# Kernel optimization log

Hardware: AMD Instinct MI355X
Metric: run time of the kernel (lower is better)

The kernel has to match this reference:

```python
import jax, jax.numpy as jnp
import numpy as np

B, S, H = 1, 2048, 4096
NH, NKV, HD = 32, 8, 128
GROUP = 128
NEG = jnp.float32(-1e9)


def setup_inputs() -> dict:
    key = jax.random.key(0)
    ks = jax.random.split(key, 13)
    inp = {"hidden_states": jax.random.normal(ks[0], (B, S, H), dtype=jnp.float32)}

    def qparams(k1, k2, k3, out_dim, in_dim):
        qw = jax.random.randint(k1, (out_dim, in_dim), 0, 16, dtype=jnp.int32)
        sc = jax.random.uniform(k2, (out_dim, in_dim // GROUP), dtype=jnp.float32) * 0.02 + 0.001
        zp = jax.random.randint(k3, (out_dim, in_dim // GROUP), 0, 16, dtype=jnp.int32)
        return qw, sc, zp

    inp["q_qw"], inp["q_sc"], inp["q_zp"] = qparams(ks[1], ks[2], ks[3], NH * HD, H)
    inp["k_qw"], inp["k_sc"], inp["k_zp"] = qparams(ks[4], ks[5], ks[6], NKV * HD, H)
    inp["v_qw"], inp["v_sc"], inp["v_zp"] = qparams(ks[7], ks[8], ks[9], NKV * HD, H)
    inp["o_qw"], inp["o_sc"], inp["o_zp"] = qparams(ks[10], ks[11], ks[12], NH * HD, H)
    return inp


def dequant(qw, sc, zp):
    # W4A16 groupwise dequant: w = (q - zero_point) * scale, group along input dim
    out_dim, in_dim = qw.shape
    g = in_dim // sc.shape[1]
    w = (qw.reshape(out_dim, -1, g) - zp[:, :, None]).astype(jnp.float32) * sc[:, :, None]
    return w.reshape(out_dim, in_dim)


def reference(hidden_states, q_qw, q_sc, q_zp, k_qw, k_sc, k_zp,
              v_qw, v_sc, v_zp, o_qw, o_sc, o_zp):
    x = hidden_states  # [B, S, H]
    grp = NH // NKV  # GQA groups = 4

    q = jnp.einsum('bsh,oh->bso', x, dequant(q_qw, q_sc, q_zp))
    k = jnp.einsum('bsh,oh->bso', x, dequant(k_qw, k_sc, k_zp))
    v = jnp.einsum('bsh,oh->bso', x, dequant(v_qw, v_sc, v_zp))

    # [B, NKV, grp, S, HD] for q; [B, NKV, S, HD] for k, v (avoid repeat_kv materialization)
    q = q.reshape(B, S, NKV, grp, HD).transpose(0, 2, 3, 1, 4)
    k = k.reshape(B, S, NKV, HD).transpose(0, 2, 1, 3)
    v = v.reshape(B, S, NKV, HD).transpose(0, 2, 1, 3)

    scale = 1.0 / jnp.sqrt(jnp.float32(HD))
    scores = jnp.einsum('bngqd,bnkd->bngqk', q, k) * scale  # [B,NKV,grp,S,S]
    causal = jnp.tril(jnp.ones((S, S), dtype=bool))
    scores = jnp.where(causal[None, None, None], scores, NEG)
    probs = jax.nn.softmax(scores, axis=-1)
    attn = jnp.einsum('bngqk,bnkd->bngqd', probs, v)  # [B,NKV,grp,S,HD]

    attn = attn.transpose(0, 3, 1, 2, 4).reshape(B, S, NH * HD)
    out = jnp.einsum('bso,ho->bsh', attn, dequant(o_qw, o_sc, o_zp).T.T) if False else jnp.einsum('bsf,of->bso', attn, dequant(o_qw, o_sc, o_zp))
    return out
```

## Files before the change

kernel.cpp:

```cpp
#include <hip/hip_runtime.h>
#include <stdint.h>

#define DI __device__ __forceinline__

typedef __attribute__((ext_vector_type(8))) _Float16 f16x8;
typedef __attribute__((ext_vector_type(4))) float f32x4;
typedef __attribute__((ext_vector_type(4))) int   i32x4;
typedef __attribute__((ext_vector_type(4))) float fvec4;
typedef __attribute__((ext_vector_type(8))) unsigned short u16x8;
typedef __attribute__((ext_vector_type(4))) unsigned short u16x4;

constexpr int S2   = 2048;
constexpr int NHD  = 4096;
constexpr int KVD  = 1024;
constexpr int QKVW = 6144;
constexpr float SCALE_LOG2E = 0.08838834764831845f * 1.4426950408889634f;

DI unsigned short f32_f16(float f) {
    union { _Float16 h; unsigned short u; } v;
    v.h = (_Float16)f;
    return v.u;
}

DI f32x4 mfma16(f16x8 a, f16x8 b, f32x4 c) {
    return __builtin_amdgcn_mfma_f32_16x16x32_f16(a, b, c, 0, 0, 0);
}

DI void load_lds16(const void* g, void* l) {
    __builtin_amdgcn_global_load_lds(
        (const __attribute__((address_space(1))) void*)(uintptr_t)g,
        (__attribute__((address_space(3))) void*)(uintptr_t)l, 16, 0, 0);
}

__global__ __launch_bounds__(256) void k_cast(const float* __restrict__ in,
                                              unsigned short* __restrict__ out) {
    int i = (blockIdx.x * 256 + threadIdx.x) * 4;
    fvec4 v = *(const fvec4*)(in + i);
    u16x4 o;
#pragma unroll
    for (int j = 0; j < 4; ++j) o[j] = f32_f16(v[j]);
    *(u16x4*)(out + i) = o;
}

__global__ __launch_bounds__(256) void k_prep(const int* __restrict__ qw,
                                              const float* __restrict__ sc,
                                              const int* __restrict__ zp,
                                              unsigned short* __restrict__ outW) {
    long long t = (long long)blockIdx.x * 256 + threadIdx.x;
    long long base = t * 8;
    int n = (int)(base >> 12);
    int g = (int)((base >> 7) & 31);
    float s = sc[n * 32 + g];
    int   z = zp[n * 32 + g];
    i32x4 a = *(const i32x4*)(qw + base);
    i32x4 b = *(const i32x4*)(qw + base + 4);
    u16x8 o;
#pragma unroll
    for (int j = 0; j < 4; ++j) {
        o[j]     = f32_f16((float)(a[j] - z) * s);
        o[4 + j] = f32_f16((float)(b[j] - z) * s);
    }
    *(u16x8*)(outW + base) = o;
}

template <typename CT, int NREP>
__global__ __launch_bounds__(512) void k_gemm8(const unsigned short* __restrict__ A,
                                               const unsigned short* __restrict__ B,
                                               CT* __restrict__ C, int N) {
    constexpr int K = 4096, BK = 32, NT = K / BK;
    constexpr int BN = NREP * 64;
    __shared__ __align__(16) unsigned short Al[3][256 * 32];
    __shared__ __align__(16) unsigned short Bl[3][BN * 32];
    const int nbx = N / BN;
    const int tot = nbx * (int)gridDim.y;
    const int h   = (int)blockIdx.x + (int)blockIdx.y * nbx;
    const int lid = (h & 7) * (tot >> 3) + (h >> 3);
    const int m0 = (lid / nbx) * 256, n0 = (lid % nbx) * BN;
    const int tid = threadIdx.x;
    const int w = tid >> 6, lane = tid & 63;
    const int wm = w >> 2, wn = w & 3;
    const int lq = lane & 15, lg = lane >> 4;
    const int cx = (lg ^ ((lq >> 1) & 3)) << 3;
    const int srow = lane >> 2;
    const int gc = (((lane & 3) ^ ((lane >> 3) & 3)) << 3);
    f32x4 acc[8][NREP] = {};

    auto stage = [&](int k0, int sl) {
#pragma unroll
        for (int j = 0; j < 2; ++j)
            load_lds16(A + (long long)(m0 + (j * 8 + w) * 16 + srow) * K + k0 + gc,
                       &Al[sl][(j * 8 + w) * 512]);
        if constexpr (NREP == 4) {
#pragma unroll
            for (int j = 0; j < 2; ++j)
                load_lds16(B + (long long)(n0 + (j * 8 + w) * 16 + srow) * K + k0 + gc,
                           &Bl[sl][(j * 8 + w) * 512]);
        } else {
            load_lds16(B + (long long)(n0 + w * 16 + srow) * K + k0 + gc,
                       &Bl[sl][w * 512]);
        }
    };

    stage(0, 0);
    stage(BK, 1);
    int cs = 0, ss = 2;
    for (int kt = 0; kt < NT; ++kt) {
        if (kt < NT - 1) {
            if constexpr (NREP == 4) asm volatile("s_waitcnt vmcnt(4)" ::: "memory");
            else                     asm volatile("s_waitcnt vmcnt(3)" ::: "memory");
        } else {
            asm volatile("s_waitcnt vmcnt(0)" ::: "memory");
        }
        __builtin_amdgcn_s_barrier();
        __builtin_amdgcn_sched_barrier(0);
        if (kt + 2 < NT) stage((kt + 2) * BK, ss);
        f16x8 af[8], bf[NREP];
#pragma unroll
        for (int i = 0; i < 8; ++i)
            af[i] = *(const f16x8*)(&Al[cs][(wm * 128 + i * 16 + lq) * 32 + cx]);
#pragma unroll
        for (int i = 0; i < NREP; ++i)
            bf[i] = *(const f16x8*)(&Bl[cs][(wn * (NREP * 16) + i * 16 + lq) * 32 + cx]);
        __builtin_amdgcn_s_setprio(1);
#pragma unroll
        for (int mi = 0; mi < 8; ++mi)
#pragma unroll
            for (int ni = 0; ni < NREP; ++ni)
                acc[mi][ni] = mfma16(af[mi], bf[ni], acc[mi][ni]);
        __builtin_amdgcn_s_setprio(0);
        __builtin_amdgcn_sched_barrier(0);
        if (++cs == 3) cs = 0;
        if (++ss == 3) ss = 0;
    }
#pragma unroll
    for (int mi = 0; mi < 8; ++mi)
#pragma unroll
        for (int ni = 0; ni < NREP; ++ni)
#pragma unroll
            for (int r = 0; r < 4; ++r) {
                const int row = m0 + wm * 128 + mi * 16 + lg * 4 + r;
                const int col = n0 + wn * (NREP * 16) + ni * 16 + lq;
                const float v = acc[mi][ni][r];
                if constexpr (sizeof(CT) == 2) C[(long long)row * N + col] = (CT)f32_f16(v);
                else                           C[(long long)row * N + col] = v;
            }
}

__global__ __launch_bounds__(256) void k_transpose_v(const unsigned short* __restrict__ QKV,
                                                     unsigned short* __restrict__ VT) {
    __shared__ unsigned short tile[32][33];
    const int s0 = blockIdx.x * 32, d0 = blockIdx.y * 32, hk = blockIdx.z;
    const int tx = threadIdx.x & 31, ty = threadIdx.x >> 5;
#pragma unroll
    for (int j = 0; j < 4; ++j)
        tile[ty + j * 8][tx] =
            QKV[(long long)(s0 + ty + j * 8) * QKVW + (NHD + KVD) + hk * 128 + d0 + tx];
    __syncthreads();
#pragma unroll
    for (int j = 0; j < 4; ++j)
        VT[((long long)hk * 128 + d0 + ty + j * 8) * S2 + s0 + tx] = tile[tx][ty + j * 8];
}

__global__ __launch_bounds__(256, 4) void k_attn(const unsigned short* __restrict__ QKV,
                                                 const unsigned short* __restrict__ VT,
                                                 unsigned short* __restrict__ O) {
    __shared__ __align__(16) unsigned short Ks[2][32 * 128];
    __shared__ __align__(16) unsigned short Vs[2][128 * 32];
    __shared__ __align__(16) unsigned short Ps[4][16 * 40];
    const int bid = blockIdx.x;
    const int hkv = bid & 7;
    const int tq  = bid >> 3;
    const int g   = (tq < 64) ? tq : 191 - tq;
    const int nt  = (g >> 1) + 1;
    const int q0  = g * 16;
    const int tid = threadIdx.x;
    const int w = tid >> 6, lane = tid & 63;
    const int lq = lane & 15, lg = lane >> 4;
    const int h = hkv * 4 + w;

    const unsigned short* Kg  = QKV + NHD + hkv * 128;
    const unsigned short* VTg = VT + (long long)hkv * 128 * S2;

    const int ksr = lane >> 4;
    const int ksc = lane & 15;
    const int vsr = lane >> 2;
    const int vsc = lane & 3;
    const int vsx = (lane >> 3) & 3;

    f16x8 qf[4];
    const unsigned short* qp = QKV + (long long)(q0 + lq) * QKVW + h * 128;
#pragma unroll
    for (int kc = 0; kc < 4; ++kc) qf[kc] = *(const f16x8*)(qp + kc * 32 + lg * 8);

    f32x4 oacc[8] = {};
    float m[4], l[4];
#pragma unroll
    for (int r = 0; r < 4; ++r) { m[r] = -1e30f; l[r] = 0.f; }

    auto stage = [&](int j0, int b) {
#pragma unroll
        for (int i = 0; i < 2; ++i) {
            const int r = 8 * w + 4 * i + ksr;
            load_lds16(Kg + (long long)(j0 + r) * QKVW + ((ksc ^ (r & 7)) << 3),
                       &Ks[b][(8 * w + 4 * i) * 128]);
        }
#pragma unroll
        for (int i = 0; i < 2; ++i) {
            const int r = 32 * w + 16 * i + vsr;
            load_lds16(VTg + (long long)r * S2 + j0 + ((vsc ^ vsx) << 3),
                       &Vs[b][(32 * w + 16 * i) * 32]);
        }
    };

    stage(0, 0);
    int buf = 0;
    for (int t = 0; t < nt; ++t) {
        const int j0 = t * 32;
        __syncthreads();
        if (t + 1 < nt) stage(j0 + 32, buf ^ 1);

        f32x4 sv[2] = {};
        __builtin_amdgcn_s_setprio(1);
#pragma unroll
        for (int kc = 0; kc < 4; ++kc)
#pragma unroll
            for (int jj = 0; jj < 2; ++jj) {
                const int c = (kc * 4 + lg) ^ (lq & 7);
                f16x8 kf = *(const f16x8*)&Ks[buf][(jj * 16 + lq) * 128 + c * 8];
                sv[jj] = mfma16(qf[kc], kf, sv[jj]);
            }
        __builtin_amdgcn_s_setprio(0);

        float t0a[4], t1a[4], pl[4];
        const bool diag = (t == nt - 1);
#pragma unroll
        for (int r = 0; r < 4; ++r) {
            float t0 = sv[0][r] * SCALE_LOG2E;
            float t1 = sv[1][r] * SCALE_LOG2E;
            if (diag) {
                const int qg = q0 + lg * 4 + r;
                if (j0 + lq > qg)      t0 = -INFINITY;
                if (j0 + 16 + lq > qg) t1 = -INFINITY;
            }
            t0a[r] = t0; t1a[r] = t1;
            pl[r] = fmaxf(t0, t1);
        }
        const bool grow = (pl[0] > m[0] + 8.f) || (pl[1] > m[1] + 8.f) ||
                          (pl[2] > m[2] + 8.f) || (pl[3] > m[3] + 8.f);
        if (__any(grow)) {
#pragma unroll
            for (int r = 0; r < 4; ++r) {
                float mx = pl[r];
                mx = fmaxf(mx, __shfl_xor(mx, 1));
                mx = fmaxf(mx, __shfl_xor(mx, 2));
                mx = fmaxf(mx, __shfl_xor(mx, 4));
                mx = fmaxf(mx, __shfl_xor(mx, 8));
                const float mn = fmaxf(m[r], mx);
                const float alpha = exp2f(m[r] - mn);
                m[r] = mn;
                l[r] *= alpha;
#pragma unroll
                for (int nb = 0; nb < 8; ++nb) oacc[nb][r] *= alpha;
            }
        }
#pragma unroll
        for (int r = 0; r < 4; ++r) {
            const float p0 = exp2f(t0a[r] - m[r]);
            const float p1 = exp2f(t1a[r] - m[r]);
            l[r] += p0 + p1;
            Ps[w][(lg * 4 + r) * 40 + lq]      = f32_f16(p0);
            Ps[w][(lg * 4 + r) * 40 + 16 + lq] = f32_f16(p1);
        }
        const f16x8 pf = *(const f16x8*)&Ps[w][lq * 40 + lg * 8];
        __builtin_amdgcn_s_setprio(1);
#pragma unroll
        for (int nb = 0; nb < 8; ++nb) {
            const int c = lg ^ ((lq >> 1) & 3);
            f16x8 vf = *(const f16x8*)&Vs[buf][(nb * 16 + lq) * 32 + c * 8];
            oacc[nb] = mfma16(pf, vf, oacc[nb]);
        }
        __builtin_amdgcn_s_setprio(0);
        buf ^= 1;
    }

    float linv[4];
#pragma unroll
    for (int r = 0; r < 4; ++r) {
        float s = l[r];
        s += __shfl_xor(s, 1);
        s += __shfl_xor(s, 2);
        s += __shfl_xor(s, 4);
        s += __shfl_xor(s, 8);
        linv[r] = 1.0f / s;
    }
#pragma unroll
    for (int nb = 0; nb < 8; ++nb)
#pragma unroll
        for (int r = 0; r < 4; ++r) {
            const int row = q0 + lg * 4 + r;
            const int col = h * 128 + nb * 16 + lq;
            O[(long long)row * NHD + col] = f32_f16(oacc[nb][r] * linv[r]);
        }
}

extern "C" void kernel_launch(void* const* d_in, const int* in_sizes, int n_in,
                              void* d_out, int out_size, void* d_ws, size_t ws_size,
                              hipStream_t stream) {
    (void)in_sizes; (void)n_in; (void)out_size; (void)ws_size;
    const float* hs  = (const float*)d_in[0];
    const int*   qqw = (const int*)d_in[1];
    const float* qsc = (const float*)d_in[2];
    const int*   qzp = (const int*)d_in[3];
    const int*   kqw = (const int*)d_in[4];
    const float* ksc = (const float*)d_in[5];
    const int*   kzp = (const int*)d_in[6];
    const int*   vqw = (const int*)d_in[7];
    const float* vsc = (const float*)d_in[8];
    const int*   vzp = (const int*)d_in[9];
    const int*   oqw = (const int*)d_in[10];
    const float* osc = (const float*)d_in[11];
    const int*   ozp = (const int*)d_in[12];

    char* ws = (char*)d_ws;
    unsigned short* x16  = (unsigned short*)(ws);
    unsigned short* wbuf = (unsigned short*)(ws + (16ULL << 20));
    unsigned short* vt   = (unsigned short*)(ws + (65ULL << 20));
    unsigned short* xatt = (unsigned short*)(ws + (69ULL << 20));
    unsigned short* qkv  = (unsigned short*)d_out;
    float* out = (float*)d_out;

    k_cast<<<8192, 256, 0, stream>>>(hs, x16);
    k_prep<<<8192, 256, 0, stream>>>(qqw, qsc, qzp, wbuf);
    k_prep<<<2048, 256, 0, stream>>>(kqw, ksc, kzp, wbuf + (size_t)4096 * 4096);
    k_prep<<<2048, 256, 0, stream>>>(vqw, vsc, vzp, wbuf + (size_t)5120 * 4096);
    k_gemm8<unsigned short, 4><<<dim3(24, 8), 512, 0, stream>>>(x16, wbuf, qkv, QKVW);
    k_transpose_v<<<dim3(64, 4, 8), 256, 0, stream>>>(qkv, vt);
    k_prep<<<8192, 256, 0, stream>>>(oqw, osc, ozp, wbuf);
    k_attn<<<1024, 256, 0, stream>>>(qkv, vt, xatt);
    k_gemm8<float, 2><<<dim3(32, 8), 512, 0, stream>>>(xatt, wbuf, out, 4096);
}
```

Measured before the change: 319.3 us.

## Retile QKV GEMM to 256x192 tiles and add 128x256 BK64 output GEMM

The QKV projection GEMM switches from 256x256 to 256x192 tiles, giving 256 blocks instead of 192 so the work spreads more evenly across the compute units. The B-tile load is split unevenly across waves, so the per-wave vmcnt wait counts differ. The output projection gets a new kernel with 128x256 tiles, BK=64, an XOR-swizzled LDS layout and 256 blocks, replacing the 256x128 BK=32 variant. The trade is more LDS per block and a different reuse ratio, in exchange for better wave quantization and fewer k-iterations.

```diff
diff --git a/kernel.cpp b/kernel.cpp
--- a/kernel.cpp
+++ b/kernel.cpp
@@ -73,8 +73,8 @@
     __shared__ __align__(16) unsigned short Bl[3][BN * 32];
     const int nbx = N / BN;
     const int tot = nbx * (int)gridDim.y;
-    const int h   = (int)blockIdx.x + (int)blockIdx.y * nbx;
-    const int lid = (h & 7) * (tot >> 3) + (h >> 3);
+    const int hg  = (int)blockIdx.x + (int)blockIdx.y * nbx;
+    const int lid = (hg & 7) * (tot >> 3) + (hg >> 3);
     const int m0 = (lid / nbx) * 256, n0 = (lid % nbx) * BN;
     const int tid = threadIdx.x;
     const int w = tid >> 6, lane = tid & 63;
@@ -95,6 +95,19 @@
             for (int j = 0; j < 2; ++j)
                 load_lds16(B + (long long)(n0 + (j * 8 + w) * 16 + srow) * K + k0 + gc,
                            &Bl[sl][(j * 8 + w) * 512]);
+        } else if constexpr (NREP == 3) {
+            if (w < 4) {
+#pragma unroll
+                for (int i = 0; i < 2; ++i) {
+                    const int r0 = w * 32 + i * 16;
+                    load_lds16(B + (long long)(n0 + r0 + srow) * K + k0 + gc,
+                               &Bl[sl][r0 * 32]);
+                }
+            } else {
+                const int r0 = 128 + (w - 4) * 16;
+                load_lds16(B + (long long)(n0 + r0 + srow) * K + k0 + gc,
+                           &Bl[sl][r0 * 32]);
+            }
         } else {
             load_lds16(B + (long long)(n0 + w * 16 + srow) * K + k0 + gc,
                        &Bl[sl][w * 512]);
@@ -106,8 +119,14 @@
     int cs = 0, ss = 2;
     for (int kt = 0; kt < NT; ++kt) {
         if (kt < NT - 1) {
-            if constexpr (NREP == 4) asm volatile("s_waitcnt vmcnt(4)" ::: "memory");
-            else                     asm volatile("s_waitcnt vmcnt(3)" ::: "memory");
+            if constexpr (NREP == 3) {
+                if (w < 4) asm volatile("s_waitcnt vmcnt(4)" ::: "memory");
+                else       asm volatile("s_waitcnt vmcnt(3)" ::: "memory");
+            } else if constexpr (NREP == 4) {
+                asm volatile("s_waitcnt vmcnt(4)" ::: "memory");
+            } else {
+                asm volatile("s_waitcnt vmcnt(3)" ::: "memory");
+            }
         } else {
             asm volatile("s_waitcnt vmcnt(0)" ::: "memory");
         }
@@ -140,6 +159,85 @@
             for (int r = 0; r < 4; ++r) {
                 const int row = m0 + wm * 128 + mi * 16 + lg * 4 + r;
                 const int col = n0 + wn * (NREP * 16) + ni * 16 + lq;
+                const float v = acc[mi][ni][r];
+                if constexpr (sizeof(CT) == 2) C[(long long)row * N + col] = (CT)f32_f16(v);
+                else                           C[(long long)row * N + col] = v;
+            }
+}
+
+template <typename CT>
+__global__ __launch_bounds__(512) void k_gemm2(const unsigned short* __restrict__ A,
+                                               const unsigned short* __restrict__ B,
+                                               CT* __restrict__ C, int N) {
+    constexpr int K = 4096, BK = 64, NT = K / BK;
+    __shared__ __align__(16) unsigned short Al[3][128 * 64];
+    __shared__ __align__(16) unsigned short Bl[3][256 * 64];
+    const int nbx = N / 256;
+    const int tot = nbx * (int)gridDim.y;
+    const int hg  = (int)blockIdx.x + (int)blockIdx.y * nbx;
+    const int lid = (hg & 7) * (tot >> 3) + (hg >> 3);
+    const int m0 = (lid / nbx) * 128, n0 = (lid % nbx) * 256;
+    const int tid = threadIdx.x;
+    const int w = tid >> 6, lane = tid & 63;
+    const int wm = w >> 2, wn = w & 3;
+    const int lq = lane & 15, lg = lane >> 4;
+    const int rsub = lane >> 3;
+    const int gch  = ((lane & 7) ^ rsub) << 3;
+    f32x4 acc[4][4] = {};
+
+    auto stage = [&](int k0, int sl) {
+#pragma unroll
+        for (int i = 0; i < 2; ++i) {
+            const int r0 = w * 16 + i * 8;
+            load_lds16(A + (long long)(m0 + r0 + rsub) * K + k0 + gch, &Al[sl][r0 * 64]);
+        }
+#pragma unroll
+        for (int i = 0; i < 4; ++i) {
+            const int r0 = w * 32 + i * 8;
+            load_lds16(B + (long long)(n0 + r0 + rsub) * K + k0 + gch, &Bl[sl][r0 * 64]);
+        }
+    };
+
+    stage(0, 0);
+    stage(BK, 1);
+    int cs = 0, ss = 2;
+    for (int kt = 0; kt < NT; ++kt) {
+        if (kt < NT - 1) asm volatile("s_waitcnt vmcnt(6)" ::: "memory");
+        else             asm volatile("s_waitcnt vmcnt(0)" ::: "memory");
+        __builtin_amdgcn_s_barrier();
+        __builtin_amdgcn_sched_barrier(0);
+        if (kt + 2 < NT) stage((kt + 2) * BK, ss);
+        f16x8 af[4][2], bf[4][2];
+#pragma unroll
+        for (int i = 0; i < 4; ++i)
+#pragma unroll
+            for (int kk = 0; kk < 2; ++kk) {
+                const int ar = wm * 64 + i * 16 + lq;
+                const int br = wn * 64 + i * 16 + lq;
+                af[i][kk] = *(const f16x8*)(&Al[cs][ar * 64 + (((kk * 4 + lg) ^ (lq & 7)) << 3)]);
+                bf[i][kk] = *(const f16x8*)(&Bl[cs][br * 64 + (((kk * 4 + lg) ^ (lq & 7)) << 3)]);
+            }
+        __builtin_amdgcn_s_setprio(1);
+#pragma unroll
+        for (int mi = 0; mi < 4; ++mi)
+#pragma unroll
+            for (int ni = 0; ni < 4; ++ni)
+#pragma unroll
+                for (int kk = 0; kk < 2; ++kk)
+                    acc[mi][ni] = mfma16(af[mi][kk], bf[ni][kk], acc[mi][ni]);
+        __builtin_amdgcn_s_setprio(0);
+        __builtin_amdgcn_sched_barrier(0);
+        if (++cs == 3) cs = 0;
+        if (++ss == 3) ss = 0;
+    }
+#pragma unroll
+    for (int mi = 0; mi < 4; ++mi)
+#pragma unroll
+        for (int ni = 0; ni < 4; ++ni)
+#pragma unroll
+            for (int r = 0; r < 4; ++r) {
+                const int row = m0 + wm * 64 + mi * 16 + lg * 4 + r;
+                const int col = n0 + wn * 64 + ni * 16 + lq;
                 const float v = acc[mi][ni][r];
                 if constexpr (sizeof(CT) == 2) C[(long long)row * N + col] = (CT)f32_f16(v);
                 else                           C[(long long)row * N + col] = v;
@@ -333,9 +431,9 @@
     k_prep<<<8192, 256, 0, stream>>>(qqw, qsc, qzp, wbuf);
     k_prep<<<2048, 256, 0, stream>>>(kqw, ksc, kzp, wbuf + (size_t)4096 * 4096);
     k_prep<<<2048, 256, 0, stream>>>(vqw, vsc, vzp, wbuf + (size_t)5120 * 4096);
-    k_gemm8<unsigned short, 4><<<dim3(24, 8), 512, 0, stream>>>(x16, wbuf, qkv, QKVW);
+    k_gemm8<unsigned short, 3><<<dim3(32, 8), 512, 0, stream>>>(x16, wbuf, qkv, QKVW);
     k_transpose_v<<<dim3(64, 4, 8), 256, 0, stream>>>(qkv, vt);
     k_prep<<<8192, 256, 0, stream>>>(oqw, osc, ozp, wbuf);
     k_attn<<<1024, 256, 0, stream>>>(qkv, vt, xatt);
-    k_gemm8<float, 2><<<dim3(32, 8), 512, 0, stream>>>(xatt, wbuf, out, 4096);
-}
+    k_gemm2<float><<<dim3(16, 16), 512, 0, stream>>>(xatt, wbuf, out, 4096);
+}
```

After: 311.2 us. 1.03x faster.
